# Optimization experiments

Measured on AMD Instinct MI355X. Metric: run time of the kernel, lower is better.

Reference implementation:

```python
import jax, jax.numpy as jnp
import numpy as np

D = 8           # spatial size of conv feature map
K = 24          # conv channels
Q = 128         # question embedding size
IN_SIZE = 2 * (K + 2) + Q  # 180
HID = 256
OUT = 28


def _coords(d):
    # faithful to torch float-tensor arithmetic: a/d is float division
    a = jnp.arange(d * d, dtype=jnp.float32)
    cx = (a / d - d / 2) / (d / 2.0)
    cy = (a % d - d / 2) / (d / 2.0)
    return jnp.stack([cx, cy], axis=1)  # [d^2, 2]


def setup_inputs() -> dict:
    key = jax.random.key(0)
    ks = jax.random.split(key, 16)
    s = 0.05
    inp = {
        "x": jax.random.normal(ks[0], (64, K, D, D), dtype=jnp.float32),
        "qst": jax.random.normal(ks[1], (64, Q), dtype=jnp.float32),
        # g MLP (weights stored [in, out])
        "g1_w": jax.random.normal(ks[2], (IN_SIZE, HID), dtype=jnp.float32) * s,
        "g1_b": jnp.zeros((HID,), dtype=jnp.float32),
        "g2_w": jax.random.normal(ks[3], (HID, HID), dtype=jnp.float32) * s,
        "g2_b": jnp.zeros((HID,), dtype=jnp.float32),
        "g3_w": jax.random.normal(ks[4], (HID, HID), dtype=jnp.float32) * s,
        "g3_b": jnp.zeros((HID,), dtype=jnp.float32),
        "g4_w": jax.random.normal(ks[5], (HID, HID), dtype=jnp.float32) * s,
        "g4_b": jnp.zeros((HID,), dtype=jnp.float32),
        # f MLP
        "f1_w": jax.random.normal(ks[6], (HID, HID), dtype=jnp.float32) * s,
        "f1_b": jnp.zeros((HID,), dtype=jnp.float32),
        "f2_w": jax.random.normal(ks[7], (HID, HID), dtype=jnp.float32) * s,
        "f2_b": jnp.zeros((HID,), dtype=jnp.float32),
        "f3_w": jax.random.normal(ks[8], (HID, OUT), dtype=jnp.float32) * s,
        "f3_b": jnp.zeros((OUT,), dtype=jnp.float32),
    }
    return inp


def _forward(x, qst, g1_w, g1_b, g2_w, g2_b, g3_w, g3_b, g4_w, g4_b,
             f1_w, f1_b, f2_w, f2_b, f3_w, f3_b):
    b, k, d, _ = x.shape
    n = d * d  # 64 objects
    # [b, n, k] object features + 2 coord channels -> [b, n, 26]
    xf = jnp.transpose(x.reshape(b, k, n), (0, 2, 1))
    ct = jnp.broadcast_to(_coords(d)[None], (b, n, 2))
    xf = jnp.concatenate([xf, ct], axis=2)                      # [b, n, 26]
    obj = k + 2
    # x_i: varies along axis 2 (original torch layout); x_j varies along axis 1 and carries qst
    xi = jnp.broadcast_to(xf[:, None, :, :], (b, n, n, obj))
    xjq = jnp.concatenate(
        [xf, jnp.broadcast_to(qst[:, None, :], (b, n, qst.shape[1]))], axis=2)
    xj = jnp.broadcast_to(xjq[:, :, None, :], (b, n, n, obj + qst.shape[1]))
    pair = jnp.concatenate([xi, xj], axis=3)                    # [b, n, n, 180]
    # g MLP over all pairs
    h = jax.nn.relu(pair @ g1_w + g1_b)
    h = jax.nn.relu(h @ g2_w + g2_b)
    h = jax.nn.relu(h @ g3_w + g3_b)
    h = jax.nn.relu(h @ g4_w + g4_b)                            # [b, n, n, 256]
    xg = jnp.sum(h, axis=(1, 2))                                # sum over d^4 pairs
    # f MLP (dropout is identity in eval mode)
    xf_ = jax.nn.relu(xg @ f1_w + f1_b)
    xf_ = jax.nn.relu(xf_ @ f2_w + f2_b)
    logits = xf_ @ f3_w + f3_b
    return jax.nn.log_softmax(logits, axis=-1)


def reference(x, qst, g1_w, g1_b, g2_w, g2_b, g3_w, g3_b, g4_w, g4_b,
              f1_w, f1_b, f2_w, f2_b, f3_w, f3_b):
    return _forward(x, qst, g1_w, g1_b, g2_w, g2_b, g3_w, g3_b, g4_w, g4_b,
                    f1_w, f1_b, f2_w, f2_b, f3_w, f3_b)
```

## Files before the change

kernel.cpp:

```cpp
#include <hip/hip_runtime.h>

typedef __bf16 bf16_t;
typedef __bf16 bf16x8 __attribute__((ext_vector_type(8)));
typedef __bf16 bf16x4 __attribute__((ext_vector_type(4)));
typedef float  f32x4  __attribute__((ext_vector_type(4)));


__global__ __launch_bounds__(256) void rn_prep_kernel(
    const float* __restrict__ x, const float* __restrict__ qst,
    const float* __restrict__ g1w, const float* __restrict__ g1b,
    const float* __restrict__ g2w, const float* __restrict__ g3w,
    const float* __restrict__ g4w,
    float* __restrict__ Ap, float* __restrict__ C,
    bf16_t* __restrict__ Wt)
{
  __shared__ float T[64][65];
  int blk = blockIdx.x;
  int n   = threadIdx.x;
  if (blk < 256) {
    int b  = blk >> 2;
    int jg = (blk & 3) * 16;
    float q0 = 0.f, q1 = 0.f, q2 = 0.f, q3 = 0.f;
    const float* qb = qst + b * 128;
    #pragma unroll 4
    for (int qi = 0; qi < 128; qi += 4) {
      q0 += qb[qi + 0] * g1w[(52 + qi + 0) * 256 + n];
      q1 += qb[qi + 1] * g1w[(52 + qi + 1) * 256 + n];
      q2 += qb[qi + 2] * g1w[(52 + qi + 2) * 256 + n];
      q3 += qb[qi + 3] * g1w[(52 + qi + 3) * 256 + n];
    }
    float accQ = g1b[n] + (q0 + q1) + (q2 + q3);

    float w24 = g1w[24 * 256 + n], w25 = g1w[25 * 256 + n];
    float w50 = g1w[50 * 256 + n], w51 = g1w[51 * 256 + n];
    float accA[16], accC[16];
    #pragma unroll
    for (int t = 0; t < 16; ++t) {
      int j = jg + t;
      float cx = ((float)j * 0.125f - 4.0f) * 0.25f;
      float cy = ((float)(j & 7) - 4.0f) * 0.25f;
      accA[t] = cx * w24 + cy * w25;
      accC[t] = accQ + cx * w50 + cy * w51;
    }
    for (int c = 0; c < 24; ++c) {
      float wa = g1w[c * 256 + n];
      float wc = g1w[(26 + c) * 256 + n];
      const float* xc = x + (b * 24 + c) * 64 + jg;
      #pragma unroll
      for (int t = 0; t < 16; ++t) {
        float xv = xc[t];
        accA[t] += xv * wa;
        accC[t] += xv * wc;
      }
    }
    int jt = blk & 3;
    int itA = n >> 5, qA = (n >> 3) & 3, eA = n & 7;
    int baseA = b * 16384 + (jt * 8 + itA) * 512 + qA * 128 + eA;
    #pragma unroll
    for (int t = 0; t < 16; ++t) {
      Ap[baseA + t * 8] = accA[t];
      C[(b * 64 + jg + t) * 256 + n] = accC[t];
    }
  } else {
    int t   = blk - 256;
    int mat = t >> 4;
    int tl  = t & 15;
    int kt  = (tl & 3) * 64;
    int nt_ = (tl >> 2) * 64;
    const float* W = (mat == 0) ? g2w : (mat == 1 ? g3w : g4w);
    int lane = n & 63, w = n >> 6;
    #pragma unroll
    for (int it = 0; it < 16; ++it) {
      int kl = w * 16 + it;
      T[kl][lane] = W[(kt + kl) * 256 + nt_ + lane];
    }
    __syncthreads();
    #pragma unroll
    for (int it = 0; it < 16; ++it) {
      int nl  = w * 16 + it;
      int no  = nt_ + nl;
      int k   = kt + lane;
      int tile = no >> 4, rr = no & 15;
      int ksI  = k >> 5,  qI = (k >> 3) & 3, e = k & 7;
      int idx  = ((tile * 8 + ksI) * 64 + qI * 16 + rr) * 8 + e;
      Wt[mat * 65536 + idx] = (bf16_t)T[lane][nl];
    }
  }
}

#define SOFTBAR()                                            \
  do {                                                       \
    asm volatile("s_waitcnt lgkmcnt(0)" ::: "memory");       \
    __builtin_amdgcn_s_barrier();                            \
    __builtin_amdgcn_sched_barrier(0);                       \
  } while (0)

__global__ __launch_bounds__(256, 2) void rn_main_kernel(
    const float* __restrict__ Ap, const float* __restrict__ C,
    const bf16_t* __restrict__ Wt,
    const float* __restrict__ g2b, const float* __restrict__ g3b,
    const float* __restrict__ g4b,
    float* __restrict__ part)
{
  __shared__ bf16_t hA[16384];
  __shared__ bf16_t hB[16384];

  int tid  = threadIdx.x;
  int bx0  = blockIdx.x;
  int bx   = (bx0 & 7) * 512 + (bx0 >> 3);
  int b    = bx >> 6;
  int i    = bx & 63;
  int lane = tid & 63;
  int wave = tid >> 6;
  int r    = lane & 15;
  int q    = lane >> 4;

  bf16x8 wf0[4];

#define PREFETCH_WF0(LL)                                                    \
  {                                                                         \
    const bf16_t* Wn = Wt + (LL) * 65536 + wave * 16384;                    \
    _Pragma("unroll")                                                       \
    for (int nt = 0; nt < 4; ++nt)                                          \
      wf0[nt] = *(const bf16x8*)&Wn[(nt * 8 * 64 + lane) * 8];              \
  }

  {
    const float* Apb = Ap + (size_t)b * 16384 + wave * 4096;
    const float* Cr  = C + ((size_t)b * 64 + i) * 256;
    #pragma unroll
    for (int it = 0; it < 8; ++it) {
      int k0 = it * 32 + q * 8;
      const float4 a0 = *(const float4*)(Apb + it * 512 + lane * 8);
      const float4 a1 = *(const float4*)(Apb + it * 512 + lane * 8 + 4);
      const float4 c0 = *(const float4*)(Cr + k0);
      const float4 c1 = *(const float4*)(Cr + k0 + 4);
      bf16x8 v;
      v[0] = (bf16_t)fmaxf(a0.x + c0.x, 0.f);
      v[1] = (bf16_t)fmaxf(a0.y + c0.y, 0.f);
      v[2] = (bf16_t)fmaxf(a0.z + c0.z, 0.f);
      v[3] = (bf16_t)fmaxf(a0.w + c0.w, 0.f);
      v[4] = (bf16_t)fmaxf(a1.x + c1.x, 0.f);
      v[5] = (bf16_t)fmaxf(a1.y + c1.y, 0.f);
      v[6] = (bf16_t)fmaxf(a1.z + c1.z, 0.f);
      v[7] = (bf16_t)fmaxf(a1.w + c1.w, 0.f);
      *(bf16x8*)&hA[((wave * 8 + it) * 64 + lane) * 8] = v;
    }
  }
  PREFETCH_WF0(0)
  SOFTBAR();

  #pragma unroll
  for (int L = 0; L < 3; ++L) {
    const bf16_t* hs = (L == 1) ? hB : hA;
    bf16_t*       hd = (L == 0) ? hB : hA;
    const bf16_t* Wl   = Wt + L * 65536 + wave * 16384;
    const float*  bias = (L == 0) ? g2b : (L == 1) ? g3b : g4b;

    f32x4 acc[4][4];
    #pragma unroll
    for (int nt = 0; nt < 4; ++nt)
      #pragma unroll
      for (int mt = 0; mt < 4; ++mt)
        #pragma unroll
        for (int e = 0; e < 4; ++e) acc[nt][mt][e] = 0.f;

    #pragma unroll
    for (int ks = 0; ks < 8; ++ks) {
      bf16x8 wf[4], hf[4];
      #pragma unroll
      for (int nt = 0; nt < 4; ++nt)
        wf[nt] = (ks == 0) ? wf0[nt]
                 : *(const bf16x8*)&Wl[((nt * 8 + ks) * 64 + lane) * 8];
      #pragma unroll
      for (int mt = 0; mt < 4; ++mt)
        hf[mt] = *(const bf16x8*)&hs[((mt * 8 + ks) * 64 + lane) * 8];
      __builtin_amdgcn_s_setprio(1);
      #pragma unroll
      for (int nt = 0; nt < 4; ++nt)
        #pragma unroll
        for (int mt = 0; mt < 4; ++mt)
          acc[nt][mt] = __builtin_amdgcn_mfma_f32_16x16x32_bf16(
              wf[nt], hf[mt], acc[nt][mt], 0, 0, 0);
      __builtin_amdgcn_s_setprio(0);
    }

    if (L < 2) {
      #pragma unroll
      for (int nt = 0; nt < 4; ++nt) {
        int k0  = wave * 64 + nt * 16 + q * 4;
        float4 bv = *(const float4*)&bias[k0];
        int ks_ = k0 >> 5, rem = k0 & 31;
        int qp  = rem >> 3, e0 = rem & 7;
        #pragma unroll
        for (int mt = 0; mt < 4; ++mt) {
          bf16x4 v;
          v[0] = (bf16_t)fmaxf(acc[nt][mt][0] + bv.x, 0.f);
          v[1] = (bf16_t)fmaxf(acc[nt][mt][1] + bv.y, 0.f);
          v[2] = (bf16_t)fmaxf(acc[nt][mt][2] + bv.z, 0.f);
          v[3] = (bf16_t)fmaxf(acc[nt][mt][3] + bv.w, 0.f);
          int off = ((mt * 8 + ks_) * 64 + qp * 16 + r) * 8 + e0;
          *(bf16x4*)&hd[off] = v;
        }
      }
      if (L == 0) PREFETCH_WF0(1)
      else        PREFETCH_WF0(2)
      SOFTBAR();
    } else {
      #pragma unroll
      for (int nt = 0; nt < 4; ++nt) {
        int k0 = wave * 64 + nt * 16 + q * 4;
        float4 bv = *(const float4*)&bias[k0];
        float p0 = 0.f, p1 = 0.f, p2 = 0.f, p3 = 0.f;
        #pragma unroll
        for (int mt = 0; mt < 4; ++mt) {
          p0 += fmaxf(acc[nt][mt][0] + bv.x, 0.f);
          p1 += fmaxf(acc[nt][mt][1] + bv.y, 0.f);
          p2 += fmaxf(acc[nt][mt][2] + bv.z, 0.f);
          p3 += fmaxf(acc[nt][mt][3] + bv.w, 0.f);
        }
        #pragma unroll
        for (int d = 1; d < 16; d <<= 1) {
          p0 += __shfl_xor(p0, d, 64);
          p1 += __shfl_xor(p1, d, 64);
          p2 += __shfl_xor(p2, d, 64);
          p3 += __shfl_xor(p3, d, 64);
        }
        if (r == 0) {
          float4 pv = make_float4(p0, p1, p2, p3);
          *(float4*)&part[(size_t)bx * 256 + k0] = pv;
        }
      }
    }
  }
#undef PREFETCH_WF0
}

__global__ __launch_bounds__(256) void rn_f_kernel(
    const float* __restrict__ part,
    const float* __restrict__ f1w, const float* __restrict__ f1b,
    const float* __restrict__ f2w, const float* __restrict__ f2b,
    const float* __restrict__ f3w, const float* __restrict__ f3b,
    float* __restrict__ out)
{
  __shared__ float xs[256], t1[256], t2[256], lg[28], lse[1];
  int b = blockIdx.x, tid = threadIdx.x;
  {
    float s0 = 0.f, s1 = 0.f, s2 = 0.f, s3 = 0.f;
    const float* pb = part + (size_t)b * 64 * 256;
    #pragma unroll 4
    for (int i = 0; i < 64; i += 4) {
      s0 += pb[(i + 0) * 256 + tid];
      s1 += pb[(i + 1) * 256 + tid];
      s2 += pb[(i + 2) * 256 + tid];
      s3 += pb[(i + 3) * 256 + tid];
    }
    xs[tid] = (s0 + s1) + (s2 + s3);
  }
  __syncthreads();
  {
    float a0 = 0.f, a1 = 0.f, a2 = 0.f, a3 = 0.f;
    for (int k = 0; k < 256; k += 4) {
      a0 += xs[k + 0] * f1w[(k + 0) * 256 + tid];
      a1 += xs[k + 1] * f1w[(k + 1) * 256 + tid];
      a2 += xs[k + 2] * f1w[(k + 2) * 256 + tid];
      a3 += xs[k + 3] * f1w[(k + 3) * 256 + tid];
    }
    t1[tid] = fmaxf(f1b[tid] + (a0 + a1) + (a2 + a3), 0.f);
  }
  __syncthreads();
  {
    float a0 = 0.f, a1 = 0.f, a2 = 0.f, a3 = 0.f;
    for (int k = 0; k < 256; k += 4) {
      a0 += t1[k + 0] * f2w[(k + 0) * 256 + tid];
      a1 += t1[k + 1] * f2w[(k + 1) * 256 + tid];
      a2 += t1[k + 2] * f2w[(k + 2) * 256 + tid];
      a3 += t1[k + 3] * f2w[(k + 3) * 256 + tid];
    }
    t2[tid] = fmaxf(f2b[tid] + (a0 + a1) + (a2 + a3), 0.f);
  }
  __syncthreads();
  if (tid < 28) {
    float a0 = 0.f, a1 = 0.f, a2 = 0.f, a3 = 0.f;
    for (int k = 0; k < 256; k += 4) {
      a0 += t2[k + 0] * f3w[(k + 0) * 28 + tid];
      a1 += t2[k + 1] * f3w[(k + 1) * 28 + tid];
      a2 += t2[k + 2] * f3w[(k + 2) * 28 + tid];
      a3 += t2[k + 3] * f3w[(k + 3) * 28 + tid];
    }
    lg[tid] = f3b[tid] + (a0 + a1) + (a2 + a3);
  }
  __syncthreads();
  if (tid == 0) {
    float m = lg[0];
    for (int j = 1; j < 28; ++j) m = fmaxf(m, lg[j]);
    float se = 0.f;
    for (int j = 0; j < 28; ++j) se += expf(lg[j] - m);
    lse[0] = m + logf(se);
  }
  __syncthreads();
  if (tid < 28) out[b * 28 + tid] = lg[tid] - lse[0];
}

extern "C" void kernel_launch(void* const* d_in, const int* in_sizes, int n_in,
                              void* d_out, int out_size, void* d_ws, size_t ws_size,
                              hipStream_t stream) {
  (void)in_sizes; (void)n_in; (void)out_size; (void)ws_size;
  const float* x   = (const float*)d_in[0];
  const float* qst = (const float*)d_in[1];
  const float* g1w = (const float*)d_in[2];
  const float* g1b = (const float*)d_in[3];
  const float* g2w = (const float*)d_in[4];
  const float* g2b = (const float*)d_in[5];
  const float* g3w = (const float*)d_in[6];
  const float* g3b = (const float*)d_in[7];
  const float* g4w = (const float*)d_in[8];
  const float* g4b = (const float*)d_in[9];
  const float* f1w = (const float*)d_in[10];
  const float* f1b = (const float*)d_in[11];
  const float* f2w = (const float*)d_in[12];
  const float* f2b = (const float*)d_in[13];
  const float* f3w = (const float*)d_in[14];
  const float* f3b = (const float*)d_in[15];
  float* out = (float*)d_out;

  float*  Ap   = (float*)d_ws;
  float*  C    = Ap + 4096 * 256;
  bf16_t* Wt   = (bf16_t*)(C + 4096 * 256);
  float*  part = (float*)((char*)Wt + 3 * 65536 * sizeof(bf16_t));

  rn_prep_kernel<<<256 + 48, 256, 0, stream>>>(
      x, qst, g1w, g1b, g2w, g3w, g4w, Ap, C, Wt);
  rn_main_kernel<<<4096, 256, 0, stream>>>(Ap, C, Wt, g2b, g3b, g4b, part);
  rn_f_kernel<<<64, 256, 0, stream>>>(part, f1w, f1b, f2w, f2b, f3w, f3b, out);
}
```

Measured before the change: 220.7 us.

## Process two i-rows per block and overlap next row's input build with epilogue

Each main-kernel block now handles two object rows i instead of one, halving the grid to 2048 blocks. The layer-1 activation tile for the second row is built into the free LDS buffer during the first row's final epilogue, and partial sums for both rows are accumulated in registers before a single store. The f-kernel reduction reads half as many partials. This amortizes per-block setup and weight prefetch and hides the build loads behind compute, at the cost of fewer blocks to spread across CUs and some extra live registers.

New measurement: 220.4 us. About the same (-0.1%).

```diff
diff --git a/kernel.cpp b/kernel.cpp
--- a/kernel.cpp
+++ b/kernel.cpp
@@ -107,9 +107,9 @@
 
   int tid  = threadIdx.x;
   int bx0  = blockIdx.x;
-  int bx   = (bx0 & 7) * 512 + (bx0 >> 3);
-  int b    = bx >> 6;
-  int i    = bx & 63;
+  int bx   = (bx0 & 7) * 256 + (bx0 >> 3);
+  int b    = bx >> 5;
+  int ip   = bx & 31;
   int lane = tid & 63;
   int wave = tid >> 6;
   int r    = lane & 15;
@@ -125,115 +125,137 @@
       wf0[nt] = *(const bf16x8*)&Wn[(nt * 8 * 64 + lane) * 8];              \
   }
 
-  {
-    const float* Apb = Ap + (size_t)b * 16384 + wave * 4096;
-    const float* Cr  = C + ((size_t)b * 64 + i) * 256;
-    #pragma unroll
-    for (int it = 0; it < 8; ++it) {
-      int k0 = it * 32 + q * 8;
-      const float4 a0 = *(const float4*)(Apb + it * 512 + lane * 8);
-      const float4 a1 = *(const float4*)(Apb + it * 512 + lane * 8 + 4);
-      const float4 c0 = *(const float4*)(Cr + k0);
-      const float4 c1 = *(const float4*)(Cr + k0 + 4);
-      bf16x8 v;
-      v[0] = (bf16_t)fmaxf(a0.x + c0.x, 0.f);
-      v[1] = (bf16_t)fmaxf(a0.y + c0.y, 0.f);
-      v[2] = (bf16_t)fmaxf(a0.z + c0.z, 0.f);
-      v[3] = (bf16_t)fmaxf(a0.w + c0.w, 0.f);
-      v[4] = (bf16_t)fmaxf(a1.x + c1.x, 0.f);
-      v[5] = (bf16_t)fmaxf(a1.y + c1.y, 0.f);
-      v[6] = (bf16_t)fmaxf(a1.z + c1.z, 0.f);
-      v[7] = (bf16_t)fmaxf(a1.w + c1.w, 0.f);
-      *(bf16x8*)&hA[((wave * 8 + it) * 64 + lane) * 8] = v;
-    }
-  }
+#define BUILD(DST, IOFF)                                                    \
+  {                                                                         \
+    const float* Apb = Ap + (size_t)b * 16384 + wave * 4096;                \
+    const float* Cr  = C + ((size_t)b * 64 + ip * 2 + (IOFF)) * 256;        \
+    _Pragma("unroll")                                                       \
+    for (int it = 0; it < 8; ++it) {                                        \
+      int k0 = it * 32 + q * 8;                                             \
+      const float4 a0 = *(const float4*)(Apb + it * 512 + lane * 8);        \
+      const float4 a1 = *(const float4*)(Apb + it * 512 + lane * 8 + 4);    \
+      const float4 c0 = *(const float4*)(Cr + k0);                          \
+      const float4 c1 = *(const float4*)(Cr + k0 + 4);                      \
+      bf16x8 v;                                                             \
+      v[0] = (bf16_t)fmaxf(a0.x + c0.x, 0.f);                               \
+      v[1] = (bf16_t)fmaxf(a0.y + c0.y, 0.f);                               \
+      v[2] = (bf16_t)fmaxf(a0.z + c0.z, 0.f);                               \
+      v[3] = (bf16_t)fmaxf(a0.w + c0.w, 0.f);                               \
+      v[4] = (bf16_t)fmaxf(a1.x + c1.x, 0.f);                               \
+      v[5] = (bf16_t)fmaxf(a1.y + c1.y, 0.f);                               \
+      v[6] = (bf16_t)fmaxf(a1.z + c1.z, 0.f);                               \
+      v[7] = (bf16_t)fmaxf(a1.w + c1.w, 0.f);                               \
+      *(bf16x8*)&(DST)[((wave * 8 + it) * 64 + lane) * 8] = v;              \
+    }                                                                       \
+  }
+
+  float4 pr[4];
+  #pragma unroll
+  for (int nt = 0; nt < 4; ++nt) pr[nt] = make_float4(0.f, 0.f, 0.f, 0.f);
+
   PREFETCH_WF0(0)
+  BUILD(hA, 0)
   SOFTBAR();
 
   #pragma unroll
-  for (int L = 0; L < 3; ++L) {
-    const bf16_t* hs = (L == 1) ? hB : hA;
-    bf16_t*       hd = (L == 0) ? hB : hA;
-    const bf16_t* Wl   = Wt + L * 65536 + wave * 16384;
-    const float*  bias = (L == 0) ? g2b : (L == 1) ? g3b : g4b;
-
-    f32x4 acc[4][4];
-    #pragma unroll
-    for (int nt = 0; nt < 4; ++nt)
-      #pragma unroll
-      for (int mt = 0; mt < 4; ++mt)
-        #pragma unroll
-        for (int e = 0; e < 4; ++e) acc[nt][mt][e] = 0.f;
-
-    #pragma unroll
-    for (int ks = 0; ks < 8; ++ks) {
-      bf16x8 wf[4], hf[4];
+  for (int ii = 0; ii < 2; ++ii) {
+    #pragma unroll
+    for (int L = 0; L < 3; ++L) {
+      const bf16_t* hs;
+      bf16_t*       hd;
+      if (ii == 0) { hs = (L == 1) ? hB : hA; hd = (L == 0) ? hB : hA; }
+      else         { hs = (L == 1) ? hA : hB; hd = (L == 0) ? hA : hB; }
+      const bf16_t* Wl   = Wt + L * 65536 + wave * 16384;
+      const float*  bias = (L == 0) ? g2b : (L == 1) ? g3b : g4b;
+
+      f32x4 acc[4][4];
       #pragma unroll
       for (int nt = 0; nt < 4; ++nt)
-        wf[nt] = (ks == 0) ? wf0[nt]
-                 : *(const bf16x8*)&Wl[((nt * 8 + ks) * 64 + lane) * 8];
+        #pragma unroll
+        for (int mt = 0; mt < 4; ++mt)
+          #pragma unroll
+          for (int e = 0; e < 4; ++e) acc[nt][mt][e] = 0.f;
+
       #pragma unroll
-      for (int mt = 0; mt < 4; ++mt)
-        hf[mt] = *(const bf16x8*)&hs[((mt * 8 + ks) * 64 + lane) * 8];
-      __builtin_amdgcn_s_setprio(1);
-      #pragma unroll
-      for (int nt = 0; nt < 4; ++nt)
+      for (int ks = 0; ks < 8; ++ks) {
+        bf16x8 wf[4], hf[4];
+        #pragma unroll
+        for (int nt = 0; nt < 4; ++nt)
+          wf[nt] = (ks == 0) ? wf0[nt]
+                   : *(const bf16x8*)&Wl[((nt * 8 + ks) * 64 + lane) * 8];
         #pragma unroll
         for (int mt = 0; mt < 4; ++mt)
-          acc[nt][mt] = __builtin_amdgcn_mfma_f32_16x16x32_bf16(
-              wf[nt], hf[mt], acc[nt][mt], 0, 0, 0);
-      __builtin_amdgcn_s_setprio(0);
-    }
-
-    if (L < 2) {
-      #pragma unroll
-      for (int nt = 0; nt < 4; ++nt) {
-        int k0  = wave * 64 + nt * 16 + q * 4;
-        float4 bv = *(const float4*)&bias[k0];
-        int ks_ = k0 >> 5, rem = k0 & 31;
-        int qp  = rem >> 3, e0 = rem & 7;
-        #pragma unroll
-        for (int mt = 0; mt < 4; ++mt) {
-          bf16x4 v;
-          v[0] = (bf16_t)fmaxf(acc[nt][mt][0] + bv.x, 0.f);
-          v[1] = (bf16_t)fmaxf(acc[nt][mt][1] + bv.y, 0.f);
-          v[2] = (bf16_t)fmaxf(acc[nt][mt][2] + bv.z, 0.f);
-          v[3] = (bf16_t)fmaxf(acc[nt][mt][3] + bv.w, 0.f);
-          int off = ((mt * 8 + ks_) * 64 + qp * 16 + r) * 8 + e0;
-          *(bf16x4*)&hd[off] = v;
+          hf[mt] = *(const bf16x8*)&hs[((mt * 8 + ks) * 64 + lane) * 8];
+        __builtin_amdgcn_s_setprio(1);
+        #pragma unroll
+        for (int nt = 0; nt < 4; ++nt)
+          #pragma unroll
+          for (int mt = 0; mt < 4; ++mt)
+            acc[nt][mt] = __builtin_amdgcn_mfma_f32_16x16x32_bf16(
+                wf[nt], hf[mt], acc[nt][mt], 0, 0, 0);
+        __builtin_amdgcn_s_setprio(0);
+      }
+
+      if (L < 2) {
+        #pragma unroll
+        for (int nt = 0; nt < 4; ++nt) {
+          int k0  = wave * 64 + nt * 16 + q * 4;
+          float4 bv = *(const float4*)&bias[k0];
+          int ks_ = k0 >> 5, rem = k0 & 31;
+          int qp  = rem >> 3, e0 = rem & 7;
+          #pragma unroll
+          for (int mt = 0; mt < 4; ++mt) {
+            bf16x4 v;
+            v[0] = (bf16_t)fmaxf(acc[nt][mt][0] + bv.x, 0.f);
+            v[1] = (bf16_t)fmaxf(acc[nt][mt][1] + bv.y, 0.f);
+            v[2] = (bf16_t)fmaxf(acc[nt][mt][2] + bv.z, 0.f);
+            v[3] = (bf16_t)fmaxf(acc[nt][mt][3] + bv.w, 0.f);
+            int off = ((mt * 8 + ks_) * 64 + qp * 16 + r) * 8 + e0;
+            *(bf16x4*)&hd[off] = v;
+          }
+        }
+        PREFETCH_WF0(L + 1)
+        SOFTBAR();
+      } else {
+        if (ii == 0) BUILD(hB, 1)
+        #pragma unroll
+        for (int nt = 0; nt < 4; ++nt) {
+          int k0 = wave * 64 + nt * 16 + q * 4;
+          float4 bv = *(const float4*)&bias[k0];
+          float p0 = 0.f, p1 = 0.f, p2 = 0.f, p3 = 0.f;
+          #pragma unroll
+          for (int mt = 0; mt < 4; ++mt) {
+            p0 += fmaxf(acc[nt][mt][0] + bv.x, 0.f);
+            p1 += fmaxf(acc[nt][mt][1] + bv.y, 0.f);
+            p2 += fmaxf(acc[nt][mt][2] + bv.z, 0.f);
+            p3 += fmaxf(acc[nt][mt][3] + bv.w, 0.f);
+          }
+          #pragma unroll
+          for (int d = 1; d < 16; d <<= 1) {
+            p0 += __shfl_xor(p0, d, 64);
+            p1 += __shfl_xor(p1, d, 64);
+            p2 += __shfl_xor(p2, d, 64);
+            p3 += __shfl_xor(p3, d, 64);
+          }
+          pr[nt].x += p0; pr[nt].y += p1; pr[nt].z += p2; pr[nt].w += p3;
+        }
+        if (ii == 0) {
+          PREFETCH_WF0(0)
+          SOFTBAR();
         }
       }
-      if (L == 0) PREFETCH_WF0(1)
-      else        PREFETCH_WF0(2)
-      SOFTBAR();
-    } else {
-      #pragma unroll
-      for (int nt = 0; nt < 4; ++nt) {
-        int k0 = wave * 64 + nt * 16 + q * 4;
-        float4 bv = *(const float4*)&bias[k0];
-        float p0 = 0.f, p1 = 0.f, p2 = 0.f, p3 = 0.f;
-        #pragma unroll
-        for (int mt = 0; mt < 4; ++mt) {
-          p0 += fmaxf(acc[nt][mt][0] + bv.x, 0.f);
-          p1 += fmaxf(acc[nt][mt][1] + bv.y, 0.f);
-          p2 += fmaxf(acc[nt][mt][2] + bv.z, 0.f);
-          p3 += fmaxf(acc[nt][mt][3] + bv.w, 0.f);
-        }
-        #pragma unroll
-        for (int d = 1; d < 16; d <<= 1) {
-          p0 += __shfl_xor(p0, d, 64);
-          p1 += __shfl_xor(p1, d, 64);
-          p2 += __shfl_xor(p2, d, 64);
-          p3 += __shfl_xor(p3, d, 64);
-        }
-        if (r == 0) {
-          float4 pv = make_float4(p0, p1, p2, p3);
-          *(float4*)&part[(size_t)bx * 256 + k0] = pv;
-        }
-      }
+    }
+  }
+
+  if (r == 0) {
+    #pragma unroll
+    for (int nt = 0; nt < 4; ++nt) {
+      int k0 = wave * 64 + nt * 16 + q * 4;
+      *(float4*)&part[(size_t)bx * 256 + k0] = pr[nt];
     }
   }
 #undef PREFETCH_WF0
+#undef BUILD
 }
 
 __global__ __launch_bounds__(256) void rn_f_kernel(
@@ -247,9 +269,9 @@
   int b = blockIdx.x, tid = threadIdx.x;
   {
     float s0 = 0.f, s1 = 0.f, s2 = 0.f, s3 = 0.f;
-    const float* pb = part + (size_t)b * 64 * 256;
+    const float* pb = part + (size_t)b * 32 * 256;
     #pragma unroll 4
-    for (int i = 0; i < 64; i += 4) {
+    for (int i = 0; i < 32; i += 4) {
       s0 += pb[(i + 0) * 256 + tid];
       s1 += pb[(i + 1) * 256 + tid];
       s2 += pb[(i + 2) * 256 + tid];
@@ -331,6 +353,6 @@
 
   rn_prep_kernel<<<256 + 48, 256, 0, stream>>>(
       x, qst, g1w, g1b, g2w, g3w, g4w, Ap, C, Wt);
-  rn_main_kernel<<<4096, 256, 0, stream>>>(Ap, C, Wt, g2b, g3b, g4b, part);
+  rn_main_kernel<<<2048, 256, 0, stream>>>(Ap, C, Wt, g2b, g3b, g4b, part);
   rn_f_kernel<<<64, 256, 0, stream>>>(part, f1w, f1b, f2w, f2b, f3w, f3b, out);
 }
```
